# Optimization experiments

Hardware: AMD Instinct MI355X
Metric: run time of the kernel (lower is better)

The kernel has to match this reference:

```python
import jax, jax.numpy as jnp
import numpy as np

NUM_SLOTS = 8
SLOT_DIM = 64
HIDDEN_DIM = 128  # max(slot_dim, 128)
ITERS = 3
EPS = 1e-08
LN_EPS = 1e-05


def _ln(x, w, b):
    mu = jnp.mean(x, axis=-1, keepdims=True)
    var = jnp.mean(jnp.square(x - mu), axis=-1, keepdims=True)
    return (x - mu) * jax.lax.rsqrt(var + LN_EPS) * w + b


def setup_inputs() -> dict:
    key = jax.random.key(0)
    ks = jax.random.split(key, 16)
    b, n, d, h, n_s = 64, 4096, SLOT_DIM, HIDDEN_DIM, NUM_SLOTS
    s = 1.0 / np.sqrt(d)
    sh = 1.0 / np.sqrt(h)
    inp = {
        'inputs': jax.random.normal(ks[0], (b, n, d), jnp.float32),
        'mask': jax.random.randint(ks[1], (b, n), 0, 2, jnp.int32),
        'noise': jax.random.normal(ks[2], (b, n_s, d), jnp.float32),
        'slots_mu': jax.random.normal(ks[3], (1, 1, d), jnp.float32),
        'slots_sigma': jax.random.uniform(ks[4], (1, 1, d), jnp.float32),
        'Wq': jax.random.normal(ks[5], (d, d), jnp.float32) * s,
        'bq': jnp.zeros((d,), jnp.float32),
        'Wk': jax.random.normal(ks[6], (d, d), jnp.float32) * s,
        'bk': jnp.zeros((d,), jnp.float32),
        'Wv': jax.random.normal(ks[7], (d, d), jnp.float32) * s,
        'bv': jnp.zeros((d,), jnp.float32),
        'W_ih': jax.random.normal(ks[8], (3 * d, d), jnp.float32) * s,
        'b_ih': jnp.zeros((3 * d,), jnp.float32),
        'W_hh': jax.random.normal(ks[9], (3 * d, d), jnp.float32) * s,
        'b_hh': jnp.zeros((3 * d,), jnp.float32),
        'W1': jax.random.normal(ks[10], (h, d), jnp.float32) * s,
        'b1': jnp.zeros((h,), jnp.float32),
        'W2': jax.random.normal(ks[11], (d, h), jnp.float32) * sh,
        'b2': jnp.zeros((d,), jnp.float32),
        'ln_in_w': jnp.ones((d,), jnp.float32), 'ln_in_b': jnp.zeros((d,), jnp.float32),
        'ln_s_w': jnp.ones((d,), jnp.float32), 'ln_s_b': jnp.zeros((d,), jnp.float32),
        'ln_ff_w': jnp.ones((d,), jnp.float32), 'ln_ff_b': jnp.zeros((d,), jnp.float32),
    }
    return inp


def reference(inputs, mask, noise, slots_mu, slots_sigma, Wq, bq, Wk, bk, Wv, bv,
              W_ih, b_ih, W_hh, b_hh, W1, b1, W2, b2,
              ln_in_w, ln_in_b, ln_s_w, ln_s_b, ln_ff_w, ln_ff_b):
    b, n, d = inputs.shape
    scale = d ** (-0.5)
    # slots ~ Normal(mu, sigma) via reparameterization with fixed noise
    slots = slots_mu + slots_sigma * noise  # [b, n_s, d]
    m = (mask[:, :, None] != 0)  # [b, n, 1]
    x = _ln(inputs, ln_in_w, ln_in_b)
    k = x @ Wk.T + bk  # [b, n, d]
    v = x @ Wv.T + bv  # [b, n, d]
    for _ in range(ITERS):
        slots_prev = slots
        s_n = _ln(slots, ln_s_w, ln_s_b)
        q = s_n @ Wq.T + bq  # [b, n_s, d]
        dots = jnp.einsum('bid,bjd->bij', k, q) * scale  # [b, n, n_s]
        attn = jax.nn.softmax(dots, axis=-1) + EPS
        attn = jnp.where(m, attn, 0.0)
        attn = attn / jnp.sum(attn, axis=-2, keepdims=True)
        updates = jnp.einsum('bij,bid->bjd', attn, v)  # [b, n_s, d]
        # GRUCell(updates, slots_prev)
        gx = updates @ W_ih.T + b_ih  # [b, n_s, 3d]
        gh = slots_prev @ W_hh.T + b_hh
        xr, xz, xn = jnp.split(gx, 3, axis=-1)
        hr, hz, hn = jnp.split(gh, 3, axis=-1)
        r = jax.nn.sigmoid(xr + hr)
        z = jax.nn.sigmoid(xz + hz)
        nn_ = jnp.tanh(xn + r * hn)
        slots = (1.0 - z) * nn_ + z * slots_prev
        # residual MLP
        ff = _ln(slots, ln_ff_w, ln_ff_b)
        slots = slots + (jax.nn.relu(ff @ W1.T + b1) @ W2.T + b2)
    return slots
```

## Files before the change

kernel.cpp:

```cpp
#include <hip/hip_runtime.h>
#include <hip/hip_bf16.h>

typedef unsigned short u16;
typedef unsigned int u32;
typedef unsigned long long u64;

#define BB 64
#define NN 4096
#define DD 64
#define NSLOT 8
#define HH 128
#define NITER 3

#define BF16_ONES_PROBE 0x3F803F80u

#define OFF_WQ   0
#define OFF_WK   4096
#define OFF_WV   8192
#define OFF_WIH  12288
#define OFF_WHH  24576
#define OFF_W1   36864
#define OFF_W2   45056
#define OFF_BQ   53248
#define OFF_BK   53312
#define OFF_BV   53376
#define OFF_BIH  53440
#define OFF_BHH  53632
#define OFF_B1   53824
#define OFF_B2   53952
#define OFF_LIW  54016
#define OFF_LIB  54080
#define OFF_LSW  54144
#define OFF_LSB  54208
#define OFF_LFW  54272
#define OFF_LFB  54336
#define OFF_WKT  54400
#define OFF_PK   58496

__device__ __forceinline__ float bf2f(u16 u) {
    union { u32 i; float f; } c; c.i = ((u32)u) << 16; return c.f;
}
__device__ __forceinline__ u16 f2bf(float f) {
    __hip_bfloat16 h = __float2bfloat16(f);
    return *reinterpret_cast<u16*>(&h);
}
__device__ __forceinline__ float ldf(const void* p, int i, bool isbf) {
    return isbf ? bf2f(((const u16*)p)[i]) : ((const float*)p)[i];
}

__device__ __forceinline__ float wsum64(float x) {
    #pragma unroll
    for (int o = 32; o > 0; o >>= 1) x += __shfl_xor(x, o);
    return x;
}

__device__ __forceinline__ float ln64(float v, const float* __restrict__ g,
                                      const float* __restrict__ b, int lane) {
    float mu = wsum64(v) * (1.f / 64.f);
    float d = v - mu;
    float var = wsum64(d * d) * (1.f / 64.f);
    return d * rsqrtf(var + 1e-5f) * g[lane] + b[lane];
}

__device__ __forceinline__ float mat64p(float xv, const float* __restrict__ P, int lane) {
    const float4* p4 = (const float4*)P;
    float acc = 0.f;
    #pragma unroll
    for (int c = 0; c < 16; c++) {
        float4 w = p4[c * 64 + lane];
        acc += w.x * __shfl(xv, 4 * c + 0) + w.y * __shfl(xv, 4 * c + 1)
             + w.z * __shfl(xv, 4 * c + 2) + w.w * __shfl(xv, 4 * c + 3);
    }
    return acc;
}

struct ConvArgs {
    const void* src[20];
    int off[20];
    int n[20];
};

__global__ __launch_bounds__(256) void conv_w(ConvArgs a, float* __restrict__ wf,
                                              const u32* __restrict__ probe) {
    bool isbf = (*probe == BF16_ONES_PROBE);
    int t = blockIdx.y;
    int idx = blockIdx.x * 256 + threadIdx.x;
    if (idx < a.n[t]) wf[a.off[t] + idx] = ldf(a.src[t], idx, isbf);
}

__global__ __launch_bounds__(256) void transp_wk(float* __restrict__ wf) {
    int idx = blockIdx.x * 256 + threadIdx.x;
    int i = idx >> 6, j = idx & 63;
    wf[OFF_WKT + i * 64 + j] = wf[OFF_WK + j * 64 + i];
}

__global__ __launch_bounds__(256) void repack_w(float* __restrict__ wf) {
    const int srcs[13] = {OFF_WV, OFF_WQ, OFF_WKT,
                          OFF_WIH, OFF_WIH + 4096, OFF_WIH + 8192,
                          OFF_WHH, OFF_WHH + 4096, OFF_WHH + 8192,
                          OFF_W1, OFF_W1 + 4096,
                          OFF_W2, OFF_W2 + 64};
    const int strd[13] = {64, 64, 64, 64, 64, 64, 64, 64, 64, 64, 64, 128, 128};
    int idx = blockIdx.x * 256 + threadIdx.x;
    if (idx >= 13 * 4096) return;
    int blk = idx >> 12, r = idx & 4095;
    int c = r >> 8, rem = r & 255, j = rem >> 2, d = rem & 3;
    wf[OFF_PK + idx] = wf[srcs[blk] + j * strd[blk] + 4 * c + d];
}

__device__ __forceinline__ void emit_qstate(
        float qv, int b, int s, int bs, int lane, const float* __restrict__ wf,
        float* __restrict__ gqp, float* __restrict__ Avec, float* __restrict__ Cvec) {
    float qkv = mat64p(qv, wf + OFF_PK + 2 * 4096, lane);
    float g_in = wf[OFF_LIW + lane];
    float b_in = wf[OFF_LIB + lane];
    float gqv = g_in * qkv;
    gqp[(b << 9) + (lane >> 2) * 32 + s * 4 + (lane & 3)] = gqv;
    float A  = wsum64(gqv);
    float bd = wsum64(qv * wf[OFF_BK + lane]);
    float cq = wsum64(b_in * qkv);
    if (lane == 0) { Avec[bs] = A; Cvec[bs] = cq + bd; }
}

__global__ __launch_bounds__(64) void init_slots(
        const void* __restrict__ noise, const void* __restrict__ mu, const void* __restrict__ sg,
        const float* __restrict__ wf, float* __restrict__ slots,
        float* __restrict__ gqp, float* __restrict__ Avec, float* __restrict__ Cvec,
        float* __restrict__ acc1, float* __restrict__ ssv, float* __restrict__ A2v,
        const u32* __restrict__ probe) {
    bool isbf = (*probe == BF16_ONES_PROBE);
    int bs = blockIdx.x;
    int b = bs >> 3, s = bs & 7;
    int i = threadIdx.x;
    int idx = bs * DD + i;
    float sl = ldf(mu, i, isbf) + ldf(sg, i, isbf) * ldf(noise, idx, isbf);
    slots[idx] = sl;
    acc1[idx] = 0.f;
    if (i == 0) { ssv[bs] = 0.f; A2v[bs] = 0.f; }
    float sn = ln64(sl, wf + OFF_LSW, wf + OFF_LSB, i);
    float qv = wf[OFF_BQ + i] + mat64p(sn, wf + OFF_PK + 1 * 4096, i);
    emit_qstate(qv, b, s, bs, i, wf, gqp, Avec, Cvec);
}

__global__ __launch_bounds__(256) void fused_attn(
        const void* __restrict__ xin, const int* __restrict__ mask,
        const float* __restrict__ gqp, const float* __restrict__ Avec,
        const float* __restrict__ Cvec,
        float* __restrict__ acc1, float* __restrict__ ssv, float* __restrict__ A2v,
        const u32* __restrict__ probe) {
    __shared__ float aw_lds[256][12];
    __shared__ float racc[4][NSLOT][64];
    __shared__ float rss[4][NSLOT];
    __shared__ float rA2[4][NSLOT];
    __shared__ u64 wmask[4];

    bool isbf = (*probe == BF16_ONES_PROBE);
    int b = blockIdx.x >> 4;
    int base = (blockIdx.x & 15) << 8;
    int tid = threadIdx.x;
    int wave = tid >> 6, lane = tid & 63;

    size_t gt = ((size_t)b << 12) + base + tid;
    int mk = mask[gt];
    float sum = 0.f, sq = 0.f;
    float d[8] = {0.f, 0.f, 0.f, 0.f, 0.f, 0.f, 0.f, 0.f};
    const float4* gq4 = (const float4*)(gqp + ((size_t)b << 9));
    if (mk) {
        if (isbf) {
            const ushort4* xr = (const ushort4*)((const u16*)xin + gt * 64);
            #pragma unroll
            for (int c = 0; c < 16; c++) {
                ushort4 u = xr[c];
                float x0 = bf2f(u.x), x1 = bf2f(u.y), x2 = bf2f(u.z), x3 = bf2f(u.w);
                sum += x0 + x1 + x2 + x3;
                sq += x0 * x0 + x1 * x1 + x2 * x2 + x3 * x3;
                #pragma unroll
                for (int s = 0; s < 8; s++) {
                    float4 q = gq4[c * 8 + s];
                    d[s] += q.x * x0 + q.y * x1 + q.z * x2 + q.w * x3;
                }
            }
        } else {
            const float4* xr = (const float4*)((const float*)xin + gt * 64);
            #pragma unroll
            for (int c = 0; c < 16; c++) {
                float4 xv = xr[c];
                sum += xv.x + xv.y + xv.z + xv.w;
                sq += xv.x * xv.x + xv.y * xv.y + xv.z * xv.z + xv.w * xv.w;
                #pragma unroll
                for (int s = 0; s < 8; s++) {
                    float4 q = gq4[c * 8 + s];
                    d[s] += q.x * xv.x + q.y * xv.y + q.z * xv.z + q.w * xv.w;
                }
            }
        }
    }
    float muv = sum * (1.f / 64.f);
    float var = sq * (1.f / 64.f) - muv * muv;
    float rs = rsqrtf(var + 1e-5f);
    const float* Av = Avec + (b << 3);
    const float* Cv = Cvec + (b << 3);
    #pragma unroll
    for (int s = 0; s < 8; s++)
        d[s] = 0.125f * (rs * d[s] - rs * muv * Av[s] + Cv[s]);

    float mx = d[0];
    #pragma unroll
    for (int s = 1; s < 8; s++) mx = fmaxf(mx, d[s]);
    float den = 0.f;
    #pragma unroll
    for (int s = 0; s < 8; s++) { d[s] = expf(d[s] - mx); den += d[s]; }
    float inv = 1.f / den;
    float attn[8], aw[8];
    #pragma unroll
    for (int s = 0; s < 8; s++) {
        attn[s] = (mk != 0) ? (d[s] * inv + 1e-8f) : 0.f;
        aw[s] = attn[s] * rs;
    }
    {
        float4 w0; w0.x = aw[0]; w0.y = aw[1]; w0.z = aw[2]; w0.w = aw[3];
        float4 w1; w1.x = aw[4]; w1.y = aw[5]; w1.z = aw[6]; w1.w = aw[7];
        *(float4*)&aw_lds[tid][0] = w0;
        *(float4*)&aw_lds[tid][4] = w1;
    }
    u64 bal = __ballot(mk != 0);
    if (lane == 0) wmask[wave] = bal;
    #pragma unroll
    for (int s = 0; s < 8; s++) {
        float t1 = wsum64(attn[s]);
        float t2 = wsum64(aw[s] * muv);
        if (lane == 0) { rss[wave][s] = t1; rA2[wave][s] = t2; }
    }
    __syncthreads();

    u64 bits = wmask[wave];
    float acc[8] = {0.f, 0.f, 0.f, 0.f, 0.f, 0.f, 0.f, 0.f};
    size_t rowbase = ((size_t)b << 12) + base + (wave << 6);
    #pragma unroll 4
    for (int t = 0; t < 64; t++) {
        if ((bits >> t) & 1ULL) {
            float xv = isbf ? bf2f(((const u16*)xin)[(rowbase + t) * 64 + lane])
                            : ((const float*)xin)[(rowbase + t) * 64 + lane];
            const float4* ap = (const float4*)&aw_lds[(wave << 6) + t][0];
            float4 a0 = ap[0], a1 = ap[1];
            acc[0] += a0.x * xv; acc[1] += a0.y * xv; acc[2] += a0.z * xv; acc[3] += a0.w * xv;
            acc[4] += a1.x * xv; acc[5] += a1.y * xv; acc[6] += a1.z * xv; acc[7] += a1.w * xv;
        }
    }
    #pragma unroll
    for (int s = 0; s < 8; s++) racc[wave][s][lane] = acc[s];
    __syncthreads();
    if (wave == 0) {
        float* ag = acc1 + ((size_t)b << 9);
        #pragma unroll
        for (int s = 0; s < 8; s++) {
            float v = racc[0][s][lane] + racc[1][s][lane] + racc[2][s][lane] + racc[3][s][lane];
            atomicAdd(ag + s * 64 + lane, v);
        }
        if (lane < NSLOT) {
            float t1 = rss[0][lane] + rss[1][lane] + rss[2][lane] + rss[3][lane];
            float t2 = rA2[0][lane] + rA2[1][lane] + rA2[2][lane] + rA2[3][lane];
            atomicAdd(ssv + (b << 3) + lane, t1);
            atomicAdd(A2v + (b << 3) + lane, t2);
        }
    }
}

__global__ __launch_bounds__(64) void finalize_k(
        const float* __restrict__ wf, float* __restrict__ acc1, float* __restrict__ ssv,
        float* __restrict__ A2v, float* __restrict__ slots,
        float* __restrict__ gqp, float* __restrict__ Avec, float* __restrict__ Cvec,
        void* __restrict__ out, int last, const u32* __restrict__ probe) {
    bool isbf = (*probe == BF16_ONES_PROBE);
    int bs = blockIdx.x;
    int b = bs >> 3, s = bs & 7;
    int i = threadIdx.x;
    int idx = bs * DD + i;
    const float* P = wf + OFF_PK;

    float sm = ssv[bs];
    float a2 = A2v[bs];
    float ac = acc1[idx];
    acc1[idx] = 0.f;
    if (i == 0) { ssv[bs] = 0.f; A2v[bs] = 0.f; }

    float un = wf[OFF_LIW + i] * (ac - a2) / sm + wf[OFF_LIB + i];

    float uv = wf[OFF_BV + i] + mat64p(un, P + 0 * 4096, i);

    float sp = slots[idx];

    float gxr = wf[OFF_BIH + i], gxz = wf[OFF_BIH + 64 + i], gxn = wf[OFF_BIH + 128 + i];
    float ghr = wf[OFF_BHH + i], ghz = wf[OFF_BHH + 64 + i], ghn = wf[OFF_BHH + 128 + i];
    const float4* pxr = (const float4*)(P + 3 * 4096);
    const float4* pxz = (const float4*)(P + 4 * 4096);
    const float4* pxn = (const float4*)(P + 5 * 4096);
    const float4* phr = (const float4*)(P + 6 * 4096);
    const float4* phz = (const float4*)(P + 7 * 4096);
    const float4* phn = (const float4*)(P + 8 * 4096);
    #pragma unroll
    for (int c = 0; c < 16; c++) {
        float u0 = __shfl(uv, 4 * c + 0), u1 = __shfl(uv, 4 * c + 1);
        float u2 = __shfl(uv, 4 * c + 2), u3 = __shfl(uv, 4 * c + 3);
        float p0 = __shfl(sp, 4 * c + 0), p1 = __shfl(sp, 4 * c + 1);
        float p2 = __shfl(sp, 4 * c + 2), p3 = __shfl(sp, 4 * c + 3);
        float4 a;
        a = pxr[c * 64 + i]; gxr += a.x * u0 + a.y * u1 + a.z * u2 + a.w * u3;
        a = pxz[c * 64 + i]; gxz += a.x * u0 + a.y * u1 + a.z * u2 + a.w * u3;
        a = pxn[c * 64 + i]; gxn += a.x * u0 + a.y * u1 + a.z * u2 + a.w * u3;
        a = phr[c * 64 + i]; ghr += a.x * p0 + a.y * p1 + a.z * p2 + a.w * p3;
        a = phz[c * 64 + i]; ghz += a.x * p0 + a.y * p1 + a.z * p2 + a.w * p3;
        a = phn[c * 64 + i]; ghn += a.x * p0 + a.y * p1 + a.z * p2 + a.w * p3;
    }
    float r = 1.f / (1.f + expf(-(gxr + ghr)));
    float z = 1.f / (1.f + expf(-(gxz + ghz)));
    float nn = tanhf(gxn + r * ghn);
    float snew = (1.f - z) * nn + z * sp;

    float ff = ln64(snew, wf + OFF_LFW, wf + OFF_LFB, i);
    float h1a = wf[OFF_B1 + i], h1b = wf[OFF_B1 + 64 + i];
    const float4* p1a = (const float4*)(P + 9 * 4096);
    const float4* p1b = (const float4*)(P + 10 * 4096);
    #pragma unroll
    for (int c = 0; c < 16; c++) {
        float f0 = __shfl(ff, 4 * c + 0), f1 = __shfl(ff, 4 * c + 1);
        float f2 = __shfl(ff, 4 * c + 2), f3 = __shfl(ff, 4 * c + 3);
        float4 a;
        a = p1a[c * 64 + i]; h1a += a.x * f0 + a.y * f1 + a.z * f2 + a.w * f3;
        a = p1b[c * 64 + i]; h1b += a.x * f0 + a.y * f1 + a.z * f2 + a.w * f3;
    }
    h1a = fmaxf(h1a, 0.f);
    h1b = fmaxf(h1b, 0.f);
    float o = snew + wf[OFF_B2 + i];
    const float4* p2a = (const float4*)(P + 11 * 4096);
    const float4* p2b = (const float4*)(P + 12 * 4096);
    #pragma unroll
    for (int c = 0; c < 16; c++) {
        float a0 = __shfl(h1a, 4 * c + 0), a1 = __shfl(h1a, 4 * c + 1);
        float a2_ = __shfl(h1a, 4 * c + 2), a3 = __shfl(h1a, 4 * c + 3);
        float b0 = __shfl(h1b, 4 * c + 0), b1 = __shfl(h1b, 4 * c + 1);
        float b2 = __shfl(h1b, 4 * c + 2), b3 = __shfl(h1b, 4 * c + 3);
        float4 a;
        a = p2a[c * 64 + i]; o += a.x * a0 + a.y * a1 + a.z * a2_ + a.w * a3;
        a = p2b[c * 64 + i]; o += a.x * b0 + a.y * b1 + a.z * b2 + a.w * b3;
    }

    slots[idx] = o;
    if (last) {
        if (isbf) ((u16*)out)[idx] = f2bf(o);
        else      ((float*)out)[idx] = o;
    } else {
        float sn2 = ln64(o, wf + OFF_LSW, wf + OFF_LSB, i);
        float qv = wf[OFF_BQ + i] + mat64p(sn2, P + 1 * 4096, i);
        emit_qstate(qv, b, s, bs, i, wf, gqp, Avec, Cvec);
    }
}

extern "C" void kernel_launch(void* const* d_in, const int* in_sizes, int n_in,
                              void* d_out, int out_size, void* d_ws, size_t ws_size,
                              hipStream_t stream) {
    const void* xin  = d_in[0];
    const int* mask  = (const int*)d_in[1];
    const void* noise = d_in[2];
    const void* mu    = d_in[3];
    const void* sg    = d_in[4];
    const u32* probe  = (const u32*)d_in[19];

    char* ws = (char*)d_ws;
    float* wf = (float*)ws;

    size_t o = 524288;
    float* gqp   = (float*)(ws + o); o += (size_t)BB * 512 * 4;
    float* Avec  = (float*)(ws + o); o += (size_t)BB * NSLOT * 4;
    float* Cvec  = (float*)(ws + o); o += (size_t)BB * NSLOT * 4;
    float* acc1  = (float*)(ws + o); o += (size_t)BB * NSLOT * DD * 4;
    float* ssv   = (float*)(ws + o); o += (size_t)BB * NSLOT * 4;
    float* A2v   = (float*)(ws + o); o += (size_t)BB * NSLOT * 4;
    float* slots = (float*)(ws + o); o += (size_t)BB * NSLOT * DD * 4;

    static const int widx[20] = {5, 7, 9, 11, 13, 15, 17, 6, 8, 10, 12, 14, 16, 18,
                                 19, 20, 21, 22, 23, 24};
    static const int woff[20] = {OFF_WQ, OFF_WK, OFF_WV, OFF_WIH, OFF_WHH, OFF_W1, OFF_W2,
                                 OFF_BQ, OFF_BK, OFF_BV, OFF_BIH, OFF_BHH, OFF_B1, OFF_B2,
                                 OFF_LIW, OFF_LIB, OFF_LSW, OFF_LSB, OFF_LFW, OFF_LFB};
    ConvArgs ca;
    for (int j = 0; j < 20; j++) {
        ca.src[j] = d_in[widx[j]];
        ca.off[j] = woff[j];
        ca.n[j]   = in_sizes[widx[j]];
    }
    conv_w<<<dim3(48, 20), 256, 0, stream>>>(ca, wf, probe);
    transp_wk<<<16, 256, 0, stream>>>(wf);
    repack_w<<<208, 256, 0, stream>>>(wf);
    init_slots<<<BB * NSLOT, 64, 0, stream>>>(noise, mu, sg, wf, slots,
                                              gqp, Avec, Cvec, acc1, ssv, A2v, probe);

    for (int it = 0; it < NITER; it++) {
        fused_attn<<<BB * 16, 256, 0, stream>>>(xin, mask, gqp, Avec, Cvec,
                                                acc1, ssv, A2v, probe);
        finalize_k<<<BB * NSLOT, 64, 0, stream>>>(wf, acc1, ssv, A2v, slots,
                                                  gqp, Avec, Cvec,
                                                  d_out, it == NITER - 1 ? 1 : 0, probe);
    }
}
```

Measured before the change: 283.2 us.

## Merge weight prep kernels, stage vectors in LDS, prefetch bf16 rows in attention

Three weight-preparation kernels (convert, transpose, repack) become one prep kernel that reads straight from the inputs into the packed layout. The small 64-wide matvecs in init and finalize now broadcast the input vector through shared memory instead of per-element shuffles, and use split accumulators. The attention kernel stages the per-batch query projection in LDS, prefetches bf16 input rows as 128-bit loads before computing, and unrolls the weighted-sum loop further. These target launch overhead and shuffle and load latency, at the cost of extra block barriers and more registers.

After: 272.7 us. 1.04x faster.

```diff
diff --git a/kernel.cpp b/kernel.cpp
--- a/kernel.cpp
+++ b/kernel.cpp
@@ -14,13 +14,6 @@
 
 #define BF16_ONES_PROBE 0x3F803F80u
 
-#define OFF_WQ   0
-#define OFF_WK   4096
-#define OFF_WV   8192
-#define OFF_WIH  12288
-#define OFF_WHH  24576
-#define OFF_W1   36864
-#define OFF_W2   45056
 #define OFF_BQ   53248
 #define OFF_BK   53312
 #define OFF_BV   53376
@@ -34,11 +27,16 @@
 #define OFF_LSB  54208
 #define OFF_LFW  54272
 #define OFF_LFB  54336
-#define OFF_WKT  54400
 #define OFF_PK   58496
 
 __device__ __forceinline__ float bf2f(u16 u) {
     union { u32 i; float f; } c; c.i = ((u32)u) << 16; return c.f;
+}
+__device__ __forceinline__ float bflo(u32 w) {
+    union { u32 i; float f; } c; c.i = w << 16; return c.f;
+}
+__device__ __forceinline__ float bfhi(u32 w) {
+    union { u32 i; float f; } c; c.i = w & 0xffff0000u; return c.f;
 }
 __device__ __forceinline__ u16 f2bf(float f) {
     __hip_bfloat16 h = __float2bfloat16(f);
@@ -62,56 +60,69 @@
     return d * rsqrtf(var + 1e-5f) * g[lane] + b[lane];
 }
 
-__device__ __forceinline__ float mat64p(float xv, const float* __restrict__ P, int lane) {
+__device__ __forceinline__ float mat64b(const float* __restrict__ xs,
+                                        const float* __restrict__ P, int lane) {
     const float4* p4 = (const float4*)P;
-    float acc = 0.f;
-    #pragma unroll
-    for (int c = 0; c < 16; c++) {
-        float4 w = p4[c * 64 + lane];
-        acc += w.x * __shfl(xv, 4 * c + 0) + w.y * __shfl(xv, 4 * c + 1)
-             + w.z * __shfl(xv, 4 * c + 2) + w.w * __shfl(xv, 4 * c + 3);
-    }
-    return acc;
-}
-
-struct ConvArgs {
-    const void* src[20];
-    int off[20];
-    int n[20];
+    const float4* x4 = (const float4*)xs;
+    float a0 = 0.f, a1 = 0.f, a2 = 0.f, a3 = 0.f;
+    #pragma unroll
+    for (int c = 0; c < 16; c += 4) {
+        float4 x0 = x4[c], x1 = x4[c + 1], x2 = x4[c + 2], x3 = x4[c + 3];
+        float4 w0 = p4[c * 64 + lane];
+        float4 w1 = p4[(c + 1) * 64 + lane];
+        float4 w2 = p4[(c + 2) * 64 + lane];
+        float4 w3 = p4[(c + 3) * 64 + lane];
+        a0 += w0.x * x0.x + w0.y * x0.y + w0.z * x0.z + w0.w * x0.w;
+        a1 += w1.x * x1.x + w1.y * x1.y + w1.z * x1.z + w1.w * x1.w;
+        a2 += w2.x * x2.x + w2.y * x2.y + w2.z * x2.z + w2.w * x2.w;
+        a3 += w3.x * x3.x + w3.y * x3.y + w3.z * x3.z + w3.w * x3.w;
+    }
+    return (a0 + a1) + (a2 + a3);
+}
+
+struct PrepArgs {
+    const void* w[7];
+    const void* v[13];
 };
 
-__global__ __launch_bounds__(256) void conv_w(ConvArgs a, float* __restrict__ wf,
+__global__ __launch_bounds__(256) void prep_w(PrepArgs a, float* __restrict__ wf,
                                               const u32* __restrict__ probe) {
     bool isbf = (*probe == BF16_ONES_PROBE);
-    int t = blockIdx.y;
     int idx = blockIdx.x * 256 + threadIdx.x;
-    if (idx < a.n[t]) wf[a.off[t] + idx] = ldf(a.src[t], idx, isbf);
-}
-
-__global__ __launch_bounds__(256) void transp_wk(float* __restrict__ wf) {
-    int idx = blockIdx.x * 256 + threadIdx.x;
-    int i = idx >> 6, j = idx & 63;
-    wf[OFF_WKT + i * 64 + j] = wf[OFF_WK + j * 64 + i];
-}
-
-__global__ __launch_bounds__(256) void repack_w(float* __restrict__ wf) {
-    const int srcs[13] = {OFF_WV, OFF_WQ, OFF_WKT,
-                          OFF_WIH, OFF_WIH + 4096, OFF_WIH + 8192,
-                          OFF_WHH, OFF_WHH + 4096, OFF_WHH + 8192,
-                          OFF_W1, OFF_W1 + 4096,
-                          OFF_W2, OFF_W2 + 64};
-    const int strd[13] = {64, 64, 64, 64, 64, 64, 64, 64, 64, 64, 64, 128, 128};
-    int idx = blockIdx.x * 256 + threadIdx.x;
-    if (idx >= 13 * 4096) return;
-    int blk = idx >> 12, r = idx & 4095;
-    int c = r >> 8, rem = r & 255, j = rem >> 2, d = rem & 3;
-    wf[OFF_PK + idx] = wf[srcs[blk] + j * strd[blk] + 4 * c + d];
+    if (idx < 13 * 4096) {
+        int blk = idx >> 12, r = idx & 4095;
+        int c = r >> 8, rem = r & 255, j = rem >> 2, dd = rem & 3;
+        int m = 4 * c + dd;
+        float val;
+        if      (blk == 0)  val = ldf(a.w[2], j * 64 + m, isbf);
+        else if (blk == 1)  val = ldf(a.w[0], j * 64 + m, isbf);
+        else if (blk == 2)  val = ldf(a.w[1], m * 64 + j, isbf);
+        else if (blk < 6)   val = ldf(a.w[3], ((blk - 3) * 64 + j) * 64 + m, isbf);
+        else if (blk < 9)   val = ldf(a.w[4], ((blk - 6) * 64 + j) * 64 + m, isbf);
+        else if (blk < 11)  val = ldf(a.w[5], ((blk - 9) * 64 + j) * 64 + m, isbf);
+        else                val = ldf(a.w[6], j * 128 + (blk - 11) * 64 + m, isbf);
+        wf[OFF_PK + idx] = val;
+    } else {
+        int k = idx - 13 * 4096;
+        const int voff[13] = {OFF_BQ, OFF_BK, OFF_BV, OFF_BIH, OFF_BHH, OFF_B1, OFF_B2,
+                              OFF_LIW, OFF_LIB, OFF_LSW, OFF_LSB, OFF_LFW, OFF_LFB};
+        const int vn[13]   = {64, 64, 64, 192, 192, 128, 64, 64, 64, 64, 64, 64, 64};
+        #pragma unroll
+        for (int t = 0; t < 13; t++) {
+            if (k < vn[t]) { wf[voff[t] + k] = ldf(a.v[t], k, isbf); return; }
+            k -= vn[t];
+        }
+    }
 }
 
 __device__ __forceinline__ void emit_qstate(
         float qv, int b, int s, int bs, int lane, const float* __restrict__ wf,
+        float* __restrict__ xa,
         float* __restrict__ gqp, float* __restrict__ Avec, float* __restrict__ Cvec) {
-    float qkv = mat64p(qv, wf + OFF_PK + 2 * 4096, lane);
+    __syncthreads();
+    xa[lane] = qv;
+    __syncthreads();
+    float qkv = mat64b(xa, wf + OFF_PK + 2 * 4096, lane);
     float g_in = wf[OFF_LIW + lane];
     float b_in = wf[OFF_LIB + lane];
     float gqv = g_in * qkv;
@@ -122,12 +133,13 @@
     if (lane == 0) { Avec[bs] = A; Cvec[bs] = cq + bd; }
 }
 
-__global__ __launch_bounds__(64) void init_slots(
+__global__ __launch_bounds__(64, 1) void init_slots(
         const void* __restrict__ noise, const void* __restrict__ mu, const void* __restrict__ sg,
         const float* __restrict__ wf, float* __restrict__ slots,
         float* __restrict__ gqp, float* __restrict__ Avec, float* __restrict__ Cvec,
         float* __restrict__ acc1, float* __restrict__ ssv, float* __restrict__ A2v,
         const u32* __restrict__ probe) {
+    __shared__ __align__(16) float xa[64];
     bool isbf = (*probe == BF16_ONES_PROBE);
     int bs = blockIdx.x;
     int b = bs >> 3, s = bs & 7;
@@ -138,9 +150,20 @@
     acc1[idx] = 0.f;
     if (i == 0) { ssv[bs] = 0.f; A2v[bs] = 0.f; }
     float sn = ln64(sl, wf + OFF_LSW, wf + OFF_LSB, i);
-    float qv = wf[OFF_BQ + i] + mat64p(sn, wf + OFF_PK + 1 * 4096, i);
-    emit_qstate(qv, b, s, bs, i, wf, gqp, Avec, Cvec);
-}
+    xa[i] = sn;
+    __syncthreads();
+    float qv = wf[OFF_BQ + i] + mat64b(xa, wf + OFF_PK + 1 * 4096, i);
+    emit_qstate(qv, b, s, bs, i, wf, xa, gqp, Avec, Cvec);
+}
+
+#define PROC4(xv, c) do {                                                         \
+    sum += xv.x + xv.y + xv.z + xv.w;                                             \
+    sq  += xv.x * xv.x + xv.y * xv.y + xv.z * xv.z + xv.w * xv.w;                 \
+    _Pragma("unroll")                                                             \
+    for (int s = 0; s < 8; s++) {                                                 \
+        float4 q = gq_s[(c) * 8 + s];                                             \
+        d[s] += q.x * xv.x + q.y * xv.y + q.z * xv.z + q.w * xv.w;                \
+    } } while (0)
 
 __global__ __launch_bounds__(256) void fused_attn(
         const void* __restrict__ xin, const int* __restrict__ mask,
@@ -148,7 +171,8 @@
         const float* __restrict__ Cvec,
         float* __restrict__ acc1, float* __restrict__ ssv, float* __restrict__ A2v,
         const u32* __restrict__ probe) {
-    __shared__ float aw_lds[256][12];
+    __shared__ float4 gq_s[128];
+    __shared__ float4 aw4[256][2];
     __shared__ float racc[4][NSLOT][64];
     __shared__ float rss[4][NSLOT];
     __shared__ float rA2[4][NSLOT];
@@ -160,38 +184,40 @@
     int tid = threadIdx.x;
     int wave = tid >> 6, lane = tid & 63;
 
+    if (tid < 128) gq_s[tid] = ((const float4*)(gqp + ((size_t)b << 9)))[tid];
+
     size_t gt = ((size_t)b << 12) + base + tid;
     int mk = mask[gt];
+    uint4 xrg[8];
+    if (mk && isbf) {
+        const uint4* xr = (const uint4*)((const u16*)xin + gt * 64);
+        #pragma unroll
+        for (int i = 0; i < 8; i++) xrg[i] = xr[i];
+    }
+    __syncthreads();
+
     float sum = 0.f, sq = 0.f;
     float d[8] = {0.f, 0.f, 0.f, 0.f, 0.f, 0.f, 0.f, 0.f};
-    const float4* gq4 = (const float4*)(gqp + ((size_t)b << 9));
     if (mk) {
         if (isbf) {
-            const ushort4* xr = (const ushort4*)((const u16*)xin + gt * 64);
             #pragma unroll
             for (int c = 0; c < 16; c++) {
-                ushort4 u = xr[c];
-                float x0 = bf2f(u.x), x1 = bf2f(u.y), x2 = bf2f(u.z), x3 = bf2f(u.w);
-                sum += x0 + x1 + x2 + x3;
-                sq += x0 * x0 + x1 * x1 + x2 * x2 + x3 * x3;
-                #pragma unroll
-                for (int s = 0; s < 8; s++) {
-                    float4 q = gq4[c * 8 + s];
-                    d[s] += q.x * x0 + q.y * x1 + q.z * x2 + q.w * x3;
-                }
+                u32 wa = (c & 1) ? xrg[c >> 1].z : xrg[c >> 1].x;
+                u32 wb = (c & 1) ? xrg[c >> 1].w : xrg[c >> 1].y;
+                float4 xv;
+                xv.x = bflo(wa); xv.y = bfhi(wa); xv.z = bflo(wb); xv.w = bfhi(wb);
+                PROC4(xv, c);
             }
         } else {
             const float4* xr = (const float4*)((const float*)xin + gt * 64);
             #pragma unroll
-            for (int c = 0; c < 16; c++) {
-                float4 xv = xr[c];
-                sum += xv.x + xv.y + xv.z + xv.w;
-                sq += xv.x * xv.x + xv.y * xv.y + xv.z * xv.z + xv.w * xv.w;
-                #pragma unroll
-                for (int s = 0; s < 8; s++) {
-                    float4 q = gq4[c * 8 + s];
-                    d[s] += q.x * xv.x + q.y * xv.y + q.z * xv.z + q.w * xv.w;
-                }
+            for (int cc = 0; cc < 4; cc++) {
+                float4 x0 = xr[4 * cc], x1 = xr[4 * cc + 1];
+                float4 x2 = xr[4 * cc + 2], x3 = xr[4 * cc + 3];
+                PROC4(x0, 4 * cc + 0);
+                PROC4(x1, 4 * cc + 1);
+                PROC4(x2, 4 * cc + 2);
+                PROC4(x3, 4 * cc + 3);
             }
         }
     }
@@ -220,8 +246,8 @@
     {
         float4 w0; w0.x = aw[0]; w0.y = aw[1]; w0.z = aw[2]; w0.w = aw[3];
         float4 w1; w1.x = aw[4]; w1.y = aw[5]; w1.z = aw[6]; w1.w = aw[7];
-        *(float4*)&aw_lds[tid][0] = w0;
-        *(float4*)&aw_lds[tid][4] = w1;
+        aw4[tid][0] = w0;
+        aw4[tid][1] = w1;
     }
     u64 bal = __ballot(mk != 0);
     if (lane == 0) wmask[wave] = bal;
@@ -236,13 +262,14 @@
     u64 bits = wmask[wave];
     float acc[8] = {0.f, 0.f, 0.f, 0.f, 0.f, 0.f, 0.f, 0.f};
     size_t rowbase = ((size_t)b << 12) + base + (wave << 6);
-    #pragma unroll 4
+    const u16* xb16 = (const u16*)xin + rowbase * 64 + lane;
+    const float* xf32 = (const float*)xin + rowbase * 64 + lane;
+    #pragma unroll 8
     for (int t = 0; t < 64; t++) {
         if ((bits >> t) & 1ULL) {
-            float xv = isbf ? bf2f(((const u16*)xin)[(rowbase + t) * 64 + lane])
-                            : ((const float*)xin)[(rowbase + t) * 64 + lane];
-            const float4* ap = (const float4*)&aw_lds[(wave << 6) + t][0];
-            float4 a0 = ap[0], a1 = ap[1];
+            float xv = isbf ? bf2f(xb16[t * 64]) : xf32[t * 64];
+            float4 a0 = aw4[(wave << 6) + t][0];
+            float4 a1 = aw4[(wave << 6) + t][1];
             acc[0] += a0.x * xv; acc[1] += a0.y * xv; acc[2] += a0.z * xv; acc[3] += a0.w * xv;
             acc[4] += a1.x * xv; acc[5] += a1.y * xv; acc[6] += a1.z * xv; acc[7] += a1.w * xv;
         }
@@ -266,11 +293,13 @@
     }
 }
 
-__global__ __launch_bounds__(64) void finalize_k(
+__global__ __launch_bounds__(64, 1) void finalize_k(
         const float* __restrict__ wf, float* __restrict__ acc1, float* __restrict__ ssv,
         float* __restrict__ A2v, float* __restrict__ slots,
         float* __restrict__ gqp, float* __restrict__ Avec, float* __restrict__ Cvec,
         void* __restrict__ out, int last, const u32* __restrict__ probe) {
+    __shared__ __align__(16) float xa[64];
+    __shared__ __align__(16) float xb[64];
     bool isbf = (*probe == BF16_ONES_PROBE);
     int bs = blockIdx.x;
     int b = bs >> 3, s = bs & 7;
@@ -279,71 +308,67 @@
     const float* P = wf + OFF_PK;
 
     float sm = ssv[bs];
-    float a2 = A2v[bs];
+    float a2v_ = A2v[bs];
     float ac = acc1[idx];
     acc1[idx] = 0.f;
     if (i == 0) { ssv[bs] = 0.f; A2v[bs] = 0.f; }
 
-    float un = wf[OFF_LIW + i] * (ac - a2) / sm + wf[OFF_LIB + i];
-
-    float uv = wf[OFF_BV + i] + mat64p(un, P + 0 * 4096, i);
-
+    float un = wf[OFF_LIW + i] * (ac - a2v_) / sm + wf[OFF_LIB + i];
+
+    xa[i] = un;
+    __syncthreads();
+    float uv = wf[OFF_BV + i] + mat64b(xa, P + 0 * 4096, i);
     float sp = slots[idx];
-
-    float gxr = wf[OFF_BIH + i], gxz = wf[OFF_BIH + 64 + i], gxn = wf[OFF_BIH + 128 + i];
-    float ghr = wf[OFF_BHH + i], ghz = wf[OFF_BHH + 64 + i], ghn = wf[OFF_BHH + 128 + i];
+    __syncthreads();
+    xa[i] = uv; xb[i] = sp;
+    __syncthreads();
+
+    const float4* x4a = (const float4*)xa;
+    const float4* x4b = (const float4*)xb;
     const float4* pxr = (const float4*)(P + 3 * 4096);
     const float4* pxz = (const float4*)(P + 4 * 4096);
     const float4* pxn = (const float4*)(P + 5 * 4096);
     const float4* phr = (const float4*)(P + 6 * 4096);
     const float4* phz = (const float4*)(P + 7 * 4096);
     const float4* phn = (const float4*)(P + 8 * 4096);
-    #pragma unroll
-    for (int c = 0; c < 16; c++) {
-        float u0 = __shfl(uv, 4 * c + 0), u1 = __shfl(uv, 4 * c + 1);
-        float u2 = __shfl(uv, 4 * c + 2), u3 = __shfl(uv, 4 * c + 3);
-        float p0 = __shfl(sp, 4 * c + 0), p1 = __shfl(sp, 4 * c + 1);
-        float p2 = __shfl(sp, 4 * c + 2), p3 = __shfl(sp, 4 * c + 3);
+    float xr0 = 0.f, xr1 = 0.f, xz0 = 0.f, xz1 = 0.f, xn0 = 0.f, xn1 = 0.f;
+    float hr0 = 0.f, hr1 = 0.f, hz0 = 0.f, hz1 = 0.f, hn0 = 0.f, hn1 = 0.f;
+    #pragma unroll
+    for (int c = 0; c < 16; c += 2) {
+        float4 u0 = x4a[c], u1 = x4a[c + 1];
+        float4 p0 = x4b[c], p1 = x4b[c + 1];
         float4 a;
-        a = pxr[c * 64 + i]; gxr += a.x * u0 + a.y * u1 + a.z * u2 + a.w * u3;
-        a = pxz[c * 64 + i]; gxz += a.x * u0 + a.y * u1 + a.z * u2 + a.w * u3;
-        a = pxn[c * 64 + i]; gxn += a.x * u0 + a.y * u1 + a.z * u2 + a.w * u3;
-        a = phr[c * 64 + i]; ghr += a.x * p0 + a.y * p1 + a.z * p2 + a.w * p3;
-        a = phz[c * 64 + i]; ghz += a.x * p0 + a.y * p1 + a.z * p2 + a.w * p3;
-        a = phn[c * 64 + i]; ghn += a.x * p0 + a.y * p1 + a.z * p2 + a.w * p3;
-    }
-    float r = 1.f / (1.f + expf(-(gxr + ghr)));
-    float z = 1.f / (1.f + expf(-(gxz + ghz)));
-    float nn = tanhf(gxn + r * ghn);
+        a = pxr[c * 64 + i];       xr0 += a.x * u0.x + a.y * u0.y + a.z * u0.z + a.w * u0.w;
+        a = pxr[(c + 1) * 64 + i]; xr1 += a.x * u1.x + a.y * u1.y + a.z * u1.z + a.w * u1.w;
+        a = pxz[c * 64 + i];       xz0 += a.x * u0.x + a.y * u0.y + a.z * u0.z + a.w * u0.w;
+        a = pxz[(c + 1) * 64 + i]; xz1 += a.x * u1.x + a.y * u1.y + a.z * u1.z + a.w * u1.w;
+        a = pxn[c * 64 + i];       xn0 += a.x * u0.x + a.y * u0.y + a.z * u0.z + a.w * u0.w;
+        a = pxn[(c + 1) * 64 + i]; xn1 += a.x * u1.x + a.y * u1.y + a.z * u1.z + a.w * u1.w;
+        a = phr[c * 64 + i];       hr0 += a.x * p0.x + a.y * p0.y + a.z * p0.z + a.w * p0.w;
+        a = phr[(c + 1) * 64 + i]; hr1 += a.x * p1.x + a.y * p1.y + a.z * p1.z + a.w * p1.w;
+        a = phz[c * 64 + i];       hz0 += a.x * p0.x + a.y * p0.y + a.z * p0.z + a.w * p0.w;
+        a = phz[(c + 1) * 64 + i]; hz1 += a.x * p1.x + a.y * p1.y + a.z * p1.z + a.w * p1.w;
+        a = phn[c * 64 + i];       hn0 += a.x * p0.x + a.y * p0.y + a.z * p0.z + a.w * p0.w;
+        a = phn[(c + 1) * 64 + i]; hn1 += a.x * p1.x + a.y * p1.y + a.z * p1.z + a.w * p1.w;
+    }
+    float r = 1.f / (1.f + expf(-(wf[OFF_BIH + i] + xr0 + xr1 + wf[OFF_BHH + i] + hr0 + hr1)));
+    float z = 1.f / (1.f + expf(-(wf[OFF_BIH + 64 + i] + xz0 + xz1 + wf[OFF_BHH + 64 + i] + hz0 + hz1)));
+    float nn = tanhf(wf[OFF_BIH + 128 + i] + xn0 + xn1 + r * (wf[OFF_BHH + 128 + i] + hn0 + hn1));
     float snew = (1.f - z) * nn + z * sp;
 
     float ff = ln64(snew, wf + OFF_LFW, wf + OFF_LFB, i);
-    float h1a = wf[OFF_B1 + i], h1b = wf[OFF_B1 + 64 + i];
-    const float4* p1a = (const float4*)(P + 9 * 4096);
-    const float4* p1b = (const float4*)(P + 10 * 4096);
-    #pragma unroll
-    for (int c = 0; c < 16; c++) {
-        float f0 = __shfl(ff, 4 * c + 0), f1 = __shfl(ff, 4 * c + 1);
-        float f2 = __shfl(ff, 4 * c + 2), f3 = __shfl(ff, 4 * c + 3);
-        float4 a;
-        a = p1a[c * 64 + i]; h1a += a.x * f0 + a.y * f1 + a.z * f2 + a.w * f3;
-        a = p1b[c * 64 + i]; h1b += a.x * f0 + a.y * f1 + a.z * f2 + a.w * f3;
-    }
+    __syncthreads();
+    xa[i] = ff;
+    __syncthreads();
+    float h1a = wf[OFF_B1 + i] + mat64b(xa, P + 9 * 4096, i);
+    float h1b = wf[OFF_B1 + 64 + i] + mat64b(xa, P + 10 * 4096, i);
     h1a = fmaxf(h1a, 0.f);
     h1b = fmaxf(h1b, 0.f);
-    float o = snew + wf[OFF_B2 + i];
-    const float4* p2a = (const float4*)(P + 11 * 4096);
-    const float4* p2b = (const float4*)(P + 12 * 4096);
-    #pragma unroll
-    for (int c = 0; c < 16; c++) {
-        float a0 = __shfl(h1a, 4 * c + 0), a1 = __shfl(h1a, 4 * c + 1);
-        float a2_ = __shfl(h1a, 4 * c + 2), a3 = __shfl(h1a, 4 * c + 3);
-        float b0 = __shfl(h1b, 4 * c + 0), b1 = __shfl(h1b, 4 * c + 1);
-        float b2 = __shfl(h1b, 4 * c + 2), b3 = __shfl(h1b, 4 * c + 3);
-        float4 a;
-        a = p2a[c * 64 + i]; o += a.x * a0 + a.y * a1 + a.z * a2_ + a.w * a3;
-        a = p2b[c * 64 + i]; o += a.x * b0 + a.y * b1 + a.z * b2 + a.w * b3;
-    }
+    __syncthreads();
+    xa[i] = h1a; xb[i] = h1b;
+    __syncthreads();
+    float o = snew + wf[OFF_B2 + i] + mat64b(xa, P + 11 * 4096, i)
+                                    + mat64b(xb, P + 12 * 4096, i);
 
     slots[idx] = o;
     if (last) {
@@ -351,16 +376,19 @@
         else      ((float*)out)[idx] = o;
     } else {
         float sn2 = ln64(o, wf + OFF_LSW, wf + OFF_LSB, i);
-        float qv = wf[OFF_BQ + i] + mat64p(sn2, P + 1 * 4096, i);
-        emit_qstate(qv, b, s, bs, i, wf, gqp, Avec, Cvec);
+        __syncthreads();
+        xa[i] = sn2;
+        __syncthreads();
+        float qv = wf[OFF_BQ + i] + mat64b(xa, P + 1 * 4096, i);
+        emit_qstate(qv, b, s, bs, i, wf, xa, gqp, Avec, Cvec);
     }
 }
 
 extern "C" void kernel_launch(void* const* d_in, const int* in_sizes, int n_in,
                               void* d_out, int out_size, void* d_ws, size_t ws_size,
                               hipStream_t stream) {
-    const void* xin  = d_in[0];
-    const int* mask  = (const int*)d_in[1];
+    const void* xin   = d_in[0];
+    const int* mask   = (const int*)d_in[1];
     const void* noise = d_in[2];
     const void* mu    = d_in[3];
     const void* sg    = d_in[4];
@@ -378,20 +406,18 @@
     float* A2v   = (float*)(ws + o); o += (size_t)BB * NSLOT * 4;
     float* slots = (float*)(ws + o); o += (size_t)BB * NSLOT * DD * 4;
 
-    static const int widx[20] = {5, 7, 9, 11, 13, 15, 17, 6, 8, 10, 12, 14, 16, 18,
-                                 19, 20, 21, 22, 23, 24};
-    static const int woff[20] = {OFF_WQ, OFF_WK, OFF_WV, OFF_WIH, OFF_WHH, OFF_W1, OFF_W2,
-                                 OFF_BQ, OFF_BK, OFF_BV, OFF_BIH, OFF_BHH, OFF_B1, OFF_B2,
-                                 OFF_LIW, OFF_LIB, OFF_LSW, OFF_LSB, OFF_LFW, OFF_LFB};
-    ConvArgs ca;
-    for (int j = 0; j < 20; j++) {
-        ca.src[j] = d_in[widx[j]];
-        ca.off[j] = woff[j];
-        ca.n[j]   = in_sizes[widx[j]];
-    }
-    conv_w<<<dim3(48, 20), 256, 0, stream>>>(ca, wf, probe);
-    transp_wk<<<16, 256, 0, stream>>>(wf);
-    repack_w<<<208, 256, 0, stream>>>(wf);
+    PrepArgs pa;
+    pa.w[0] = d_in[5];
+    pa.w[1] = d_in[7];
+    pa.w[2] = d_in[9];
+    pa.w[3] = d_in[11];
+    pa.w[4] = d_in[13];
+    pa.w[5] = d_in[15];
+    pa.w[6] = d_in[17];
+    static const int vidx[13] = {6, 8, 10, 12, 14, 16, 18, 19, 20, 21, 22, 23, 24};
+    for (int j = 0; j < 13; j++) pa.v[j] = d_in[vidx[j]];
+
+    prep_w<<<213, 256, 0, stream>>>(pa, wf, probe);
     init_slots<<<BB * NSLOT, 64, 0, stream>>>(noise, mu, sg, wf, slots,
                                               gqp, Avec, Cvec, acc1, ssv, A2v, probe);
 
```
